# Optimization experiments

Measured on AMD Instinct MI355X. Metric: run time of the kernel, lower is better.

## Reference

```python
import jax, jax.numpy as jnp
import numpy as np

N_DRUG, N_DIS = 3072, 3072
N = N_DRUG + N_DIS
E = 196608
F1, F2, F3 = 512, 256, 128
GAMMA1 = GAMMA2 = GAMMA3 = 0.03125
NEG_SLOPE = 0.2   # GATConv default negative_slope
KERNEL_W = 0.25   # drug_ps/dis_ps = 1/kernel_len


def gat_layer(x, src, dst, w_e, W, a_src, a_dst, b):
    """Single-head GATConv: gather -> per-node softmax -> scatter-aggregate.
    Edge weights w_e scale the unnormalized attention."""
    xw = x @ W                                                  # [N, F]
    e = jax.nn.leaky_relu((xw @ a_src)[src] + (xw @ a_dst)[dst], NEG_SLOPE)  # [E]
    m = jax.ops.segment_max(e, dst, num_segments=N)
    ex = jnp.exp(e - m[dst]) * w_e
    denom = jax.ops.segment_sum(ex, dst, num_segments=N)
    alpha = ex / (denom[dst] + 1e-16)
    out = jax.ops.segment_sum(alpha[:, None] * xw[src], dst, num_segments=N)
    return out + b


def gip_kernel(y, gamma):
    """getGipKernel(y, 0, gamma, normalized=True)."""
    mn = jnp.min(y, axis=1, keepdims=True)
    mx = jnp.max(y, axis=1, keepdims=True)
    y = (y - mn) / (mx - mn + 1e-12)          # row-wise min-max normalize
    k = y @ y.T
    k = k / jnp.mean(jnp.diagonal(k))
    d = jnp.diagonal(k)
    dist = d[:, None] + d[None, :] - 2.0 * k  # kernelToDistance
    return jnp.exp(-gamma * dist)


def normalized_kernel(K):
    K = jnp.abs(K)
    minv = jnp.min(jnp.where(K > 0, K, jnp.inf))
    K = jnp.where(K == 0, minv, K)            # replace zeros with min nonzero
    d = jnp.sqrt(jnp.diagonal(K))
    return K / (d[:, None] * d[None, :])


def setup_inputs() -> dict:
    key = jax.random.key(0)
    ks = jax.random.split(key, 20)
    f32 = jnp.float32

    def lin(k, fi, fo):
        return jax.random.normal(k, (fi, fo), f32) * (1.0 / float(np.sqrt(fi)))

    inp = {
        'x': jax.random.normal(ks[0], (N, N), f32),
        'edge_index': jax.random.randint(ks[1], (2, E), 0, N, dtype=jnp.int32),
        'adj_data': jax.random.uniform(ks[2], (N, N), f32),
        'drug_sim': jax.random.uniform(ks[3], (N_DRUG, N_DRUG), f32),
        'dis_sim': jax.random.uniform(ks[4], (N_DIS, N_DIS), f32),
        'alpha1': jax.random.normal(ks[5], (N_DRUG, N_DIS), f32),
        'alpha2': jax.random.normal(ks[6], (N_DIS, N_DRUG), f32),
        'W1': lin(ks[7], N, F1),
        'as1': jax.random.normal(ks[8], (F1,), f32) * 0.1,
        'ad1': jax.random.normal(ks[9], (F1,), f32) * 0.1,
        'b1': jnp.zeros((F1,), f32),
        'W2': lin(ks[10], F1, F2),
        'as2': jax.random.normal(ks[11], (F2,), f32) * 0.1,
        'ad2': jax.random.normal(ks[12], (F2,), f32) * 0.1,
        'b2': jnp.zeros((F2,), f32),
        'W3': lin(ks[13], F2, F3),
        'as3': jax.random.normal(ks[14], (F3,), f32) * 0.1,
        'ad3': jax.random.normal(ks[15], (F3,), f32) * 0.1,
        'b3': jnp.zeros((F3,), f32),
    }
    return inp


def reference(x, edge_index, adj_data, drug_sim, dis_sim, alpha1, alpha2,
              W1, as1, ad1, b1, W2, as2, ad2, b2, W3, as3, ad3, b3):
    src0, dst0 = edge_index[0], edge_index[1]
    w0 = adj_data[src0, dst0]                  # per-edge gather of dense weights
    loop = jnp.arange(N, dtype=src0.dtype)     # GATConv add_self_loops=True
    src = jnp.concatenate([src0, loop])
    dst = jnp.concatenate([dst0, loop])
    w = jnp.concatenate([w0, jnp.ones((N,), adj_data.dtype)])

    H1 = jax.nn.relu(gat_layer(x, src, dst, w, W1, as1, ad1, b1))
    H2 = jax.nn.relu(gat_layer(H1, src, dst, w, W2, as2, ad2, b2))
    H3 = jax.nn.relu(gat_layer(H2, src, dst, w, W3, as3, ad3, b3))

    drug_k = KERNEL_W * (gip_kernel(H1[:N_DRUG], GAMMA1)
                         + gip_kernel(H2[:N_DRUG], GAMMA2)
                         + gip_kernel(H3[:N_DRUG], GAMMA3) + drug_sim)
    dis_k = KERNEL_W * (gip_kernel(H1[N_DRUG:], GAMMA1)
                        + gip_kernel(H2[N_DRUG:], GAMMA2)
                        + gip_kernel(H3[N_DRUG:], GAMMA3) + dis_sim)

    out1 = normalized_kernel(drug_k) @ alpha1  # [N_DRUG, N_DIS]
    out2 = normalized_kernel(dis_k) @ alpha2   # [N_DIS, N_DRUG]
    return 0.5 * (out1 + out2.T)
```

## Files before the change

### kernel.cpp

```cpp
#include <hip/hip_runtime.h>
#include <hip/hip_bf16.h>
#include <stdint.h>

#define N_NODES 6144
#define N_DRUG  3072
#define N_EDGE  196608
#define E_TOT   (N_EDGE + N_NODES)
#define GAMMA   0.03125f
#define LOG2E   1.44269504f

typedef __bf16 bf16x8 __attribute__((ext_vector_type(8)));
typedef float  f32x4  __attribute__((ext_vector_type(4)));

__device__ __forceinline__ unsigned short f2b(float f){
  union { float f; unsigned u; } v; v.f = f;
  unsigned r = v.u + 0x7FFFu + ((v.u >> 16) & 1u);
  return (unsigned short)(r >> 16);
}
__device__ __forceinline__ float b2f(unsigned short b){
  union { unsigned u; float f; } v; v.u = ((unsigned)b) << 16;
  return v.f;
}
__device__ __forceinline__ float fexp2(float x){
  float r; asm("v_exp_f32 %0, %1" : "=v"(r) : "v"(x)); return r;
}
__device__ __forceinline__ void gl_lds(const void* g, void* l){
  __builtin_amdgcn_global_load_lds((const __attribute__((address_space(1))) void*)g,
                                   (__attribute__((address_space(3))) void*)l, 16, 0, 0);
}

#define WAITVM(N) asm volatile("s_waitcnt vmcnt(" #N ")" ::: "memory")
#define SYNC() { __builtin_amdgcn_sched_barrier(0); __builtin_amdgcn_s_barrier(); __builtin_amdgcn_sched_barrier(0); }

__global__ void cast_bf16_k(const float* __restrict__ in, unsigned short* __restrict__ out, long n){
  long i = ((long)blockIdx.x*blockDim.x + threadIdx.x)*4;
  long stride = (long)gridDim.x*blockDim.x*4;
  for (; i < n; i += stride){
    float4 v = *(const float4*)(in + i);
    ushort4 o;
    o.x = f2b(v.x); o.y = f2b(v.y); o.z = f2b(v.z); o.w = f2b(v.w);
    *(ushort4*)(out + i) = o;
  }
}

__global__ void tcast_k(const float* __restrict__ in, unsigned short* __restrict__ out,
                        int R, int Cd, int OLD, int OOFF){
  __shared__ float tile[32][33];
  int bx = blockIdx.x*32, by = blockIdx.y*32;
  int tx = threadIdx.x, ty = threadIdx.y;
  for (int i = ty; i < 32; i += 8) tile[i][tx] = in[(long)(by+i)*Cd + bx + tx];
  __syncthreads();
  for (int i = ty; i < 32; i += 8) out[(long)(bx+i)*OLD + OOFF + by + tx] = f2b(tile[tx][i]);
}

__global__ void tcast2_k(const float* __restrict__ a2, const float* __restrict__ a1,
                         unsigned short* __restrict__ o0, unsigned short* __restrict__ o1){
  __shared__ float tile[32][33];
  const float* in = blockIdx.z ? a1 : a2;
  unsigned short* out = blockIdx.z ? o1 : o0;
  int OOFF = blockIdx.z ? 0 : N_DRUG;
  int bx = blockIdx.x*32, by = blockIdx.y*32;
  int tx = threadIdx.x, ty = threadIdx.y;
  for (int i = ty; i < 32; i += 8) tile[i][tx] = in[(long)(by+i)*N_DRUG + bx + tx];
  __syncthreads();
  for (int i = ty; i < 32; i += 8) out[(long)(bx+i)*N_NODES + OOFF + by + tx] = f2b(tile[tx][i]);
}

__global__ void hist_k(const int* __restrict__ ei, int* __restrict__ cnt){
  int i = blockIdx.x*blockDim.x + threadIdx.x;
  if (i >= E_TOT) return;
  int d = (i < N_EDGE) ? ei[N_EDGE + i] : (i - N_EDGE);
  atomicAdd(&cnt[d], 1);
}

__global__ void scan_k(const int* __restrict__ cnt, int* __restrict__ ptr){
  __shared__ int sums[1024];
  int t = threadIdx.x;
  int v[6]; int s = 0;
  #pragma unroll
  for (int i = 0; i < 6; i++){ v[i] = s; s += cnt[t*6 + i]; }
  sums[t] = s; __syncthreads();
  for (int off = 1; off < 1024; off <<= 1){
    int add = (t >= off) ? sums[t - off] : 0;
    __syncthreads();
    sums[t] += add;
    __syncthreads();
  }
  int base = (t == 0) ? 0 : sums[t-1];
  #pragma unroll
  for (int i = 0; i < 6; i++) ptr[t*6 + i] = base + v[i];
  if (t == 1023) ptr[N_NODES] = sums[1023];
}

__global__ void scatter_k(const int* __restrict__ ei, const float* __restrict__ adj,
                          const int* __restrict__ ptr, int* __restrict__ cur,
                          int* __restrict__ srcs, int* __restrict__ dsts,
                          float* __restrict__ wcsr){
  int i = blockIdx.x*blockDim.x + threadIdx.x;
  if (i >= E_TOT) return;
  int s = (i < N_EDGE) ? ei[i] : (i - N_EDGE);
  int d = (i < N_EDGE) ? ei[N_EDGE + i] : (i - N_EDGE);
  int pos = ptr[d] + atomicAdd(&cur[d], 1);
  srcs[pos] = s; dsts[pos] = d;
  wcsr[pos] = (i < N_EDGE) ? adj[(long)s*N_NODES + d] : 1.0f;
}

__global__ void dots_k(const unsigned short* __restrict__ XWb, const float* __restrict__ av,
                       const float* __restrict__ dv, float* __restrict__ es,
                       float* __restrict__ ed, int F){
  int n = blockIdx.x, l = threadIdx.x;
  float s = 0.f, d = 0.f;
  for (int f = l*4; f < F; f += 256){
    ushort4 u = *(const ushort4*)(XWb + (long)n*F + f);
    float4 a = *(const float4*)(av + f);
    float4 dd = *(const float4*)(dv + f);
    s += b2f(u.x)*a.x + b2f(u.y)*a.y + b2f(u.z)*a.z + b2f(u.w)*a.w;
    d += b2f(u.x)*dd.x + b2f(u.y)*dd.y + b2f(u.z)*dd.z + b2f(u.w)*dd.w;
  }
  #pragma unroll
  for (int off = 32; off > 0; off >>= 1){ s += __shfl_down(s, off); d += __shfl_down(d, off); }
  if (l == 0){ es[n] = s; ed[n] = d; }
}

__global__ void phase12_k(const int* __restrict__ srcs, const int* __restrict__ dsts,
                          const float* __restrict__ wcsr,
                          const float* __restrict__ es, const float* __restrict__ ed,
                          float* __restrict__ exc){
  int p = blockIdx.x*blockDim.x + threadIdx.x;
  if (p >= E_TOT) return;
  int s = srcs[p], d = dsts[p];
  float e = es[s] + ed[d];
  e = (e > 0.f) ? e : 0.2f*e;
  exc[p] = fexp2(e * LOG2E) * wcsr[p];
}

__global__ void agg4_k(const unsigned short* __restrict__ XWb, const int* __restrict__ ptr,
                       const int* __restrict__ srcs, const float* __restrict__ exc,
                       const float* __restrict__ bias,
                       unsigned short* __restrict__ Hb, int F){
  int n = blockIdx.x, t = threadIdx.x;
  int st = ptr[n], en = ptr[n+1];
  float a0v = 0.f, a1v = 0.f, a2v = 0.f, a3v = 0.f, dsum = 0.f;
  int j = st;
  for (; j + 1 < en; j += 2){
    float w0 = exc[j], w1 = exc[j+1];
    int s0 = srcs[j], s1 = srcs[j+1];
    ushort4 u0 = *(const ushort4*)(XWb + (long)s0*F + t*4);
    ushort4 u1 = *(const ushort4*)(XWb + (long)s1*F + t*4);
    dsum += w0 + w1;
    a0v += w0*b2f(u0.x) + w1*b2f(u1.x); a1v += w0*b2f(u0.y) + w1*b2f(u1.y);
    a2v += w0*b2f(u0.z) + w1*b2f(u1.z); a3v += w0*b2f(u0.w) + w1*b2f(u1.w);
  }
  if (j < en){
    float w0 = exc[j]; int s0 = srcs[j];
    ushort4 u0 = *(const ushort4*)(XWb + (long)s0*F + t*4);
    dsum += w0;
    a0v += w0*b2f(u0.x); a1v += w0*b2f(u0.y); a2v += w0*b2f(u0.z); a3v += w0*b2f(u0.w);
  }
  float invd = 1.f/(dsum + 1e-16f);
  float4 b = *(const float4*)(bias + t*4);
  ushort4 ob;
  ob.x = f2b(fmaxf(a0v*invd + b.x, 0.f)); ob.y = f2b(fmaxf(a1v*invd + b.y, 0.f));
  ob.z = f2b(fmaxf(a2v*invd + b.z, 0.f)); ob.w = f2b(fmaxf(a3v*invd + b.w, 0.f));
  *(ushort4*)(Hb + (long)n*F + t*4) = ob;
}

__global__ void agg_k(const unsigned short* __restrict__ XWb, const int* __restrict__ ptr,
                      const int* __restrict__ srcs, const float* __restrict__ exc,
                      const float* __restrict__ bias,
                      unsigned short* __restrict__ Hb, int F){
  int n = blockIdx.x, t = threadIdx.x;
  int st = ptr[n], en = ptr[n+1];
  float ax = 0.f, ay = 0.f, dsum = 0.f;
  int j = st;
  for (; j + 1 < en; j += 2){
    float a0 = exc[j], a1 = exc[j+1];
    int s0 = srcs[j], s1 = srcs[j+1];
    ushort2 u0 = *(const ushort2*)(XWb + (long)s0*F + t*2);
    ushort2 u1 = *(const ushort2*)(XWb + (long)s1*F + t*2);
    dsum += a0 + a1;
    ax += a0*b2f(u0.x) + a1*b2f(u1.x);
    ay += a0*b2f(u0.y) + a1*b2f(u1.y);
  }
  if (j < en){
    float a = exc[j]; int s = srcs[j];
    ushort2 u = *(const ushort2*)(XWb + (long)s*F + t*2);
    dsum += a;
    ax += a*b2f(u.x); ay += a*b2f(u.y);
  }
  float invd = 1.f/(dsum + 1e-16f);
  float2 b = *(const float2*)(bias + t*2);
  ushort2 o;
  o.x = f2b(fmaxf(ax*invd + b.x, 0.f));
  o.y = f2b(fmaxf(ay*invd + b.y, 0.f));
  *(ushort2*)(Hb + (long)n*F + t*2) = o;
}

__global__ void rownorm_all_k(const unsigned short* __restrict__ H0, const unsigned short* __restrict__ H1,
                              const unsigned short* __restrict__ H2,
                              unsigned short* __restrict__ y0, unsigned short* __restrict__ y1,
                              float* __restrict__ dv0, float* __restrict__ dv1){
  int seg = blockIdx.y;
  int side = seg / 3, layer = seg % 3;
  int F = 512 >> layer;
  const unsigned short* H = (layer == 0) ? H0 : (layer == 1) ? H1 : H2;
  H += (size_t)(side ? N_DRUG : 0) * F;
  unsigned short* yb = ((side ? y1 : y0) + ((layer == 0) ? 0 : (layer == 1) ? 512 : 768));
  float* dvec = (side ? dv1 : dv0) + layer*N_DRUG;

  int r = blockIdx.x, t = threadIdx.x;
  __shared__ float ra[256], rb[256];
  float mn = 3.4e38f, mx = -3.4e38f;
  for (int f = t; f < F; f += 256){
    float v = b2f(H[(long)r*F + f]);
    mn = fminf(mn, v); mx = fmaxf(mx, v);
  }
  ra[t] = mn; rb[t] = mx; __syncthreads();
  for (int s2 = 128; s2 > 0; s2 >>= 1){
    if (t < s2){ ra[t] = fminf(ra[t], ra[t+s2]); rb[t] = fmaxf(rb[t], rb[t+s2]); }
    __syncthreads();
  }
  mn = ra[0]; mx = rb[0];
  __syncthreads();
  float sc = 1.f/(mx - mn + 1e-12f);
  float s = 0.f;
  for (int f = t; f < F; f += 256){
    float v = (b2f(H[(long)r*F + f]) - mn)*sc;
    unsigned short b = f2b(v);
    yb[(long)r*896 + f] = b;
    float vb = b2f(b);
    s += vb*vb;
  }
  ra[t] = s; __syncthreads();
  for (int s2 = 128; s2 > 0; s2 >>= 1){
    if (t < s2) ra[t] += ra[t+s2];
    __syncthreads();
  }
  if (t == 0) dvec[r] = ra[0];
}

__global__ void vsum_diag_k(const float* __restrict__ dv0, const float* __restrict__ dv1,
                            float* __restrict__ sump,
                            const float* __restrict__ sim0, const float* __restrict__ sim1,
                            float* __restrict__ rs0, float* __restrict__ rs1){
  int y = blockIdx.y;
  int t = threadIdx.x;
  if (y < 6){
    int side = y / 3, layer = y % 3;
    const float* v = (side ? dv1 : dv0) + layer*N_DRUG;
    __shared__ float red[256];
    float s = 0.f;
    for (int i = blockIdx.x*256 + t; i < N_DRUG; i += gridDim.x*256) s += v[i];
    red[t] = s; __syncthreads();
    for (int s2 = 128; s2 > 0; s2 >>= 1){ if (t < s2) red[t] += red[t+s2]; __syncthreads(); }
    if (t == 0) atomicAdd(&sump[y], red[0]);
  } else {
    int side = y - 6;
    int i = blockIdx.x*256 + t;
    const float* sim = side ? sim1 : sim0;
    float* rs = side ? rs1 : rs0;
    if (i < N_DRUG) rs[i] = rsqrtf(sim[(long)i*N_DRUG + i] + 3.0f);
  }
}

__global__ __launch_bounds__(512, 2) void gemm8p(
    const unsigned short* __restrict__ A, const unsigned short* __restrict__ Bt,
    float* __restrict__ P, float* __restrict__ Palt, int M, int N, int K, int kz)
{
  __shared__ unsigned short lds[2][2][16384];
  int t = threadIdx.x;
  int lane = t & 63, wave = t >> 6;
  int wm = wave >> 2, wn = wave & 3;

  int nbx = gridDim.x;
  int nwg = nbx * gridDim.y;
  int bid = blockIdx.y * nbx + blockIdx.x;
  int cpx = nwg >> 3;
  int swz = (bid & 7) * cpx + (bid >> 3);
  long brow = (long)(swz / nbx) * 256;
  long bcol = (long)(swz % nbx) * 256;
  long k0 = (long)blockIdx.z * kz;
  int nt = kz >> 6;

  int sr = wave*8 + (lane >> 3);
  int cg = (lane & 7) ^ (lane >> 3);
  const unsigned short* gA = A  + (brow + sr)*(long)K + k0 + cg*8;
  const unsigned short* gB = Bt + (bcol + sr)*(long)K + k0 + cg*8;
  unsigned ldsw = wave * 512;

  auto stage = [&](int b, int mat, int h, int tk){
    const unsigned short* g = (mat ? gB : gA) + (long)(h*128)*K + (long)tk*64;
    unsigned short* d = &lds[b][mat][h*8192 + ldsw];
    gl_lds(g, d);
    gl_lds(g + (long)64*K, d + 4096);
  };

  int fr = lane & 15, q = lane >> 4;
  int lo = fr*64 + ((q ^ (fr & 7))*8);
  int dk = (lo ^ 32) - lo;

  f32x4 acc[8][4];
  #pragma unroll
  for (int a = 0; a < 8; a++)
    #pragma unroll
    for (int b = 0; b < 4; b++){ acc[a][b][0]=0.f; acc[a][b][1]=0.f; acc[a][b][2]=0.f; acc[a][b][3]=0.f; }
  bf16x8 af[4][2], bf[4][2];

  const unsigned short* a0p = &lds[0][0][wm*8192 + lo];
  const unsigned short* b0p = &lds[0][1][wn*4096 + lo];
  const unsigned short* a1p = &lds[1][0][wm*8192 + lo];
  const unsigned short* b1p = &lds[1][1][wn*4096 + lo];

#define RD_AF_LO(ab) { _Pragma("unroll") for (int j = 0; j < 4; ++j){ \
    af[j][0] = *(const bf16x8*)((ab) + j*1024); af[j][1] = *(const bf16x8*)((ab) + j*1024 + dk); } }
#define RD_AF_HI(ab) { _Pragma("unroll") for (int j = 0; j < 4; ++j){ \
    af[j][0] = *(const bf16x8*)((ab) + (4+j)*1024); af[j][1] = *(const bf16x8*)((ab) + (4+j)*1024 + dk); } }
#define RD_BF_LO(bb) { _Pragma("unroll") for (int j = 0; j < 2; ++j){ \
    bf[j][0] = *(const bf16x8*)((bb) + j*1024); bf[j][1] = *(const bf16x8*)((bb) + j*1024 + dk); } }
#define RD_BF_HI(bb) { _Pragma("unroll") for (int j = 2; j < 4; ++j){ \
    bf[j][0] = *(const bf16x8*)((bb) + j*1024); bf[j][1] = *(const bf16x8*)((bb) + j*1024 + dk); } }
#define MFMA_Q(MB, NB) { __builtin_amdgcn_s_setprio(1); \
    _Pragma("unroll") for (int kk = 0; kk < 2; ++kk) \
      _Pragma("unroll") for (int mi = 0; mi < 4; ++mi) \
        _Pragma("unroll") for (int ni = (NB); ni < (NB)+2; ++ni) \
          acc[(MB)+mi][ni] = __builtin_amdgcn_mfma_f32_16x16x32_bf16(af[mi][kk], bf[ni][kk], acc[(MB)+mi][ni], 0, 0, 0); \
    __builtin_amdgcn_s_setprio(0); }

  stage(0,0,0,0); stage(0,0,1,0); stage(0,1,0,0); stage(0,1,1,0);
  stage(1,1,0,1); stage(1,1,1,1);
  WAITVM(4);
  SYNC();

  int half = nt >> 1;
  for (int i = 0; i < half; ++i){
    int t1 = 2*i+1, t2 = 2*i+2, t3 = 2*i+3;
    bool s2 = t2 < nt, s3 = t3 < nt;
    RD_AF_LO(a0p); RD_BF_LO(b0p);
    stage(1,0,0,t1);
    SYNC(); MFMA_Q(0,0); SYNC();
    RD_BF_HI(b0p);
    stage(1,0,1,t1);
    SYNC(); MFMA_Q(0,2); SYNC();
    RD_AF_HI(a0p);
    if (s2) stage(0,1,0,t2);
    SYNC(); MFMA_Q(4,0); SYNC();
    if (s2){ stage(0,1,1,t2); WAITVM(4); } else { WAITVM(0); }
    SYNC(); MFMA_Q(4,2); SYNC();
    RD_AF_LO(a1p); RD_BF_LO(b1p);
    if (s2) stage(0,0,0,t2);
    SYNC(); MFMA_Q(0,0); SYNC();
    RD_BF_HI(b1p);
    if (s2) stage(0,0,1,t2);
    SYNC(); MFMA_Q(0,2); SYNC();
    RD_AF_HI(a1p);
    if (s3) stage(1,1,0,t3);
    SYNC(); MFMA_Q(4,0); SYNC();
    if (s3){ stage(1,1,1,t3); WAITVM(4); } else { WAITVM(0); }
    SYNC(); MFMA_Q(4,2); SYNC();
  }
#undef RD_AF_LO
#undef RD_AF_HI
#undef RD_BF_LO
#undef RD_BF_HI
#undef MFMA_Q

  int z = blockIdx.z;
  float* Pz = (z < 2) ? (P + (long)z*M*N) : (Palt + (long)(z-2)*M*N);
  #pragma unroll
  for (int mi = 0; mi < 8; ++mi){
    #pragma unroll
    for (int ni = 0; ni < 4; ++ni){
      long col = bcol + wn*64 + ni*16 + fr;
      #pragma unroll
      for (int r = 0; r < 4; ++r){
        long row = brow + wm*128 + mi*16 + q*4 + r;
        Pz[row*N + col] = acc[mi][ni][r];
      }
    }
  }
}

__global__ void reduce4b_k(const float* __restrict__ p, unsigned short* __restrict__ outb, long n){
  long i = ((long)blockIdx.x*blockDim.x + threadIdx.x)*4;
  if (i >= n) return;
  float4 s = *(const float4*)(p + i);
  #pragma unroll
  for (int z = 1; z < 4; z++){
    float4 x = *(const float4*)(p + (long)z*n + i);
    s.x += x.x; s.y += x.y; s.z += x.z; s.w += x.w;
  }
  ushort4 o; o.x = f2b(s.x); o.y = f2b(s.y); o.z = f2b(s.z); o.w = f2b(s.w);
  *(ushort4*)(outb + i) = o;
}

__global__ void reduce3h_k(const float* __restrict__ pa, const float* __restrict__ pb,
                           const float* __restrict__ pc, float* __restrict__ out, long n){
  long i = ((long)blockIdx.x*blockDim.x + threadIdx.x)*4;
  if (i >= n) return;
  float4 a = *(const float4*)(pa + i);
  float4 b = *(const float4*)(pb + i);
  float4 c = *(const float4*)(pc + i);
  float4 o;
  o.x = 0.5f*(a.x + b.x + c.x); o.y = 0.5f*(a.y + b.y + c.y);
  o.z = 0.5f*(a.z + b.z + c.z); o.w = 0.5f*(a.w + b.w + c.w);
  *(float4*)(out + i) = o;
}

__global__ __launch_bounds__(256) void gemm_tn(
    const unsigned short* __restrict__ A, const unsigned short* __restrict__ Bt,
    unsigned short* __restrict__ Cb, int M, int N, int K)
{
  __shared__ unsigned short As[2][128*64];
  __shared__ unsigned short Bs[2][128*64];
  int t = threadIdx.x;
  int wave = t >> 6, lane = t & 63;
  int brow = blockIdx.y*128, bcol = blockIdx.x*128;
  int wr = (wave >> 1)*64, wc = (wave & 1)*64;
  int fr = lane & 15, q = lane >> 4;
  int rin = lane >> 3, kslot = (lane & 7) ^ rin;

  f32x4 acc[4][4];
  #pragma unroll
  for (int a = 0; a < 4; a++)
    #pragma unroll
    for (int b = 0; b < 4; b++){ acc[a][b][0]=0.f; acc[a][b][1]=0.f; acc[a][b][2]=0.f; acc[a][b][3]=0.f; }

  int aoff[4][2], boff[4][2];
  #pragma unroll
  for (int mi = 0; mi < 4; mi++){
    int row = wr + mi*16 + fr;
    #pragma unroll
    for (int kk = 0; kk < 2; kk++) aoff[mi][kk] = row*64 + (((kk*4 + q) ^ (row & 7))*8);
  }
  #pragma unroll
  for (int ni = 0; ni < 4; ni++){
    int row = wc + ni*16 + fr;
    #pragma unroll
    for (int kk = 0; kk < 2; kk++) boff[ni][kk] = row*64 + (((kk*4 + q) ^ (row & 7))*8);
  }

  auto stage = [&](int buf, int k0){
    #pragma unroll
    for (int p = 0; p < 4; p++){
      int rsec = p*32 + wave*8;
      gl_lds(A  + (long)(brow + rsec + rin)*K + k0 + kslot*8, &As[buf][rsec*64]);
      gl_lds(Bt + (long)(bcol + rsec + rin)*K + k0 + kslot*8, &Bs[buf][rsec*64]);
    }
  };

  int nsteps = K >> 6;
  stage(0, 0);
  __syncthreads();
  int curb = 0;
  for (int s = 0; s < nsteps; s++){
    if (s + 1 < nsteps) stage(curb ^ 1, (s + 1)*64);
    const unsigned short* a_l = As[curb];
    const unsigned short* b_l = Bs[curb];
    #pragma unroll
    for (int kk = 0; kk < 2; kk++){
      bf16x8 af[4], bfv[4];
      #pragma unroll
      for (int mi = 0; mi < 4; mi++) af[mi]  = *(const bf16x8*)(a_l + aoff[mi][kk]);
      #pragma unroll
      for (int ni = 0; ni < 4; ni++) bfv[ni] = *(const bf16x8*)(b_l + boff[ni][kk]);
      #pragma unroll
      for (int mi = 0; mi < 4; mi++)
        #pragma unroll
        for (int ni = 0; ni < 4; ni++)
          acc[mi][ni] = __builtin_amdgcn_mfma_f32_16x16x32_bf16(af[mi], bfv[ni], acc[mi][ni], 0, 0, 0);
    }
    __syncthreads();
    curb ^= 1;
  }

  #pragma unroll
  for (int mi = 0; mi < 4; mi++){
    #pragma unroll
    for (int ni = 0; ni < 4; ni++){
      int col = bcol + wc + ni*16 + fr;
      #pragma unroll
      for (int r = 0; r < 4; r++){
        int row = brow + wr + mi*16 + q*4 + r;
        Cb[(long)row*N + col] = f2b(acc[mi][ni][r]);
      }
    }
  }
}

__global__ __launch_bounds__(512) void gip_gemm(
    const unsigned short* __restrict__ Y0, const unsigned short* __restrict__ Y1,
    const float* __restrict__ sim0, const float* __restrict__ sim1,
    const float* __restrict__ dva, const float* __restrict__ dvb,
    const float* __restrict__ sumps,
    const float* __restrict__ rs0, const float* __restrict__ rs1,
    unsigned short* __restrict__ o0, unsigned short* __restrict__ o1)
{
  __shared__ unsigned short As[2][128*64];
  __shared__ unsigned short Bs[2][128*64];
  const int K = 896;
  int side = blockIdx.z;
  const unsigned short* Y = side ? Y1 : Y0;
  const float* sim  = side ? sim1 : sim0;
  const float* dv   = side ? dvb : dva;
  const float* sums = sumps + side*3;
  const float* rs   = side ? rs1 : rs0;
  unsigned short* outp = side ? o1 : o0;
  int outoff = side ? N_DRUG : 0;

  int t = threadIdx.x;
  int wave = t >> 6, lane = t & 63;
  int brow = blockIdx.y*128, bcol = blockIdx.x*128;
  int wr = (wave >> 1)*32, wc = (wave & 1)*64;
  int fr = lane & 15, q = lane >> 4;
  int rin = lane >> 3, kslot = (lane & 7) ^ rin;

  f32x4 acc0[2][4], acc1[2][4], acc2[2][4];
  #pragma unroll
  for (int a = 0; a < 2; a++)
    #pragma unroll
    for (int b = 0; b < 4; b++){
      acc0[a][b][0]=0.f;acc0[a][b][1]=0.f;acc0[a][b][2]=0.f;acc0[a][b][3]=0.f;
      acc1[a][b][0]=0.f;acc1[a][b][1]=0.f;acc1[a][b][2]=0.f;acc1[a][b][3]=0.f;
      acc2[a][b][0]=0.f;acc2[a][b][1]=0.f;acc2[a][b][2]=0.f;acc2[a][b][3]=0.f;
    }

  int aoff[2][2], boff[4][2];
  #pragma unroll
  for (int mi = 0; mi < 2; mi++){
    int row = wr + mi*16 + fr;
    #pragma unroll
    for (int kk = 0; kk < 2; kk++) aoff[mi][kk] = row*64 + (((kk*4 + q) ^ (row & 7))*8);
  }
  #pragma unroll
  for (int ni = 0; ni < 4; ni++){
    int row = wc + ni*16 + fr;
    #pragma unroll
    for (int kk = 0; kk < 2; kk++) boff[ni][kk] = row*64 + (((kk*4 + q) ^ (row & 7))*8);
  }

  auto stage = [&](int buf, int k0){
    #pragma unroll
    for (int p = 0; p < 2; p++){
      int rsec = p*64 + wave*8;
      gl_lds(Y + (long)(brow + rsec + rin)*K + k0 + kslot*8, &As[buf][rsec*64]);
      gl_lds(Y + (long)(bcol + rsec + rin)*K + k0 + kslot*8, &Bs[buf][rsec*64]);
    }
  };

  int curb = 0, s = 0;
  stage(0, 0);
  __syncthreads();

#define GSTEP(ACC) { \
    if (s + 1 < 14) stage(curb ^ 1, (s + 1)*64); \
    const unsigned short* a_l = As[curb]; \
    const unsigned short* b_l = Bs[curb]; \
    _Pragma("unroll") \
    for (int kk = 0; kk < 2; kk++){ \
      bf16x8 af0 = *(const bf16x8*)(a_l + aoff[0][kk]); \
      bf16x8 af1 = *(const bf16x8*)(a_l + aoff[1][kk]); \
      _Pragma("unroll") \
      for (int ni = 0; ni < 4; ni++){ \
        bf16x8 bv = *(const bf16x8*)(b_l + boff[ni][kk]); \
        ACC[0][ni] = __builtin_amdgcn_mfma_f32_16x16x32_bf16(af0, bv, ACC[0][ni], 0, 0, 0); \
        ACC[1][ni] = __builtin_amdgcn_mfma_f32_16x16x32_bf16(af1, bv, ACC[1][ni], 0, 0, 0); \
      } \
    } \
    __syncthreads(); curb ^= 1; s++; }

  for (int i = 0; i < 8; i++) GSTEP(acc0)
  for (int i = 0; i < 4; i++) GSTEP(acc1)
  for (int i = 0; i < 2; i++) GSTEP(acc2)
#undef GSTEP

  float h0 = GAMMA * ((float)N_DRUG / sums[0]) * LOG2E;
  float h1 = GAMMA * ((float)N_DRUG / sums[1]) * LOG2E;
  float h2 = GAMMA * ((float)N_DRUG / sums[2]) * LOG2E;
  float c0 = 2.f*h0, c1 = 2.f*h1, c2 = 2.f*h2;
  #pragma unroll
  for (int mi = 0; mi < 2; mi++){
    #pragma unroll
    for (int ni = 0; ni < 4; ni++){
      int col = bcol + wc + ni*16 + fr;
      float d0c = dv[col], d1c = dv[N_DRUG + col], d2c = dv[2*N_DRUG + col];
      float rc = rs[col];
      #pragma unroll
      for (int r = 0; r < 4; r++){
        int row = brow + wr + mi*16 + q*4 + r;
        float b0 = -h0*(dv[row] + d0c);
        float b1 = -h1*(dv[N_DRUG + row] + d1c);
        float b2 = -h2*(dv[2*N_DRUG + row] + d2c);
        float v = sim[(long)row*N_DRUG + col]
                + fexp2(fmaf(c0, acc0[mi][ni][r], b0))
                + fexp2(fmaf(c1, acc1[mi][ni][r], b1))
                + fexp2(fmaf(c2, acc2[mi][ni][r], b2));
        outp[(long)row*N_NODES + outoff + col] = f2b(v * rs[row] * rc);
      }
    }
  }
}

extern "C" void kernel_launch(void* const* d_in, const int* in_sizes, int n_in,
                              void* d_out, int out_size, void* d_ws, size_t ws_size,
                              hipStream_t stream){
  const float* x        = (const float*)d_in[0];
  const int*   ei       = (const int*)d_in[1];
  const float* adj      = (const float*)d_in[2];
  const float* drug_sim = (const float*)d_in[3];
  const float* dis_sim  = (const float*)d_in[4];
  const float* alpha1   = (const float*)d_in[5];
  const float* alpha2   = (const float*)d_in[6];
  const float* W[3]   = {(const float*)d_in[7],  (const float*)d_in[11], (const float*)d_in[15]};
  const float* as_[3] = {(const float*)d_in[8],  (const float*)d_in[12], (const float*)d_in[16]};
  const float* ad_[3] = {(const float*)d_in[9],  (const float*)d_in[13], (const float*)d_in[17]};
  const float* bs_[3] = {(const float*)d_in[10], (const float*)d_in[14], (const float*)d_in[18]};
  float* out = (float*)d_out;
  const int Fs[3] = {512, 256, 128};

  char* p = (char*)d_ws;
  auto alloc = [&](size_t bytes)->char*{
    char* r = p; p += (bytes + 255) & ~(size_t)255; return r;
  };
  unsigned short* xb  = (unsigned short*)alloc((size_t)N_NODES*N_NODES*2);
  unsigned short* wb  = (unsigned short*)alloc((size_t)N_NODES*512*2);
  unsigned short* XWb = (unsigned short*)alloc((size_t)N_NODES*512*2);
  unsigned short* HbL[3];
  HbL[0] = (unsigned short*)alloc((size_t)N_NODES*512*2);
  HbL[1] = (unsigned short*)alloc((size_t)N_NODES*256*2);
  HbL[2] = (unsigned short*)alloc((size_t)N_NODES*128*2);
  float* es    = (float*)alloc(N_NODES*4);
  float* edv   = (float*)alloc(N_NODES*4);
  float* exc   = (float*)alloc((size_t)E_TOT*4);
  int* cntcur  = (int*)alloc((size_t)2*N_NODES*4);
  int* cnt = cntcur, *cur = cntcur + N_NODES;
  int* cptr = (int*)alloc((N_NODES+1)*4);
  int* srcs  = (int*)alloc((size_t)E_TOT*4);
  int* dsts  = (int*)alloc((size_t)E_TOT*4);
  float* wcsr = (float*)alloc((size_t)E_TOT*4);
  unsigned short* ycat[2];
  ycat[0] = (unsigned short*)alloc((size_t)N_DRUG*896*2);
  ycat[1] = (unsigned short*)alloc((size_t)N_DRUG*896*2);
  float* dvv[2];
  dvv[0] = (float*)alloc((size_t)3*N_DRUG*4);
  dvv[1] = (float*)alloc((size_t)3*N_DRUG*4);
  float* sump = (float*)alloc(256);
  float* rsv[2];
  rsv[0] = (float*)alloc(N_DRUG*4);
  rsv[1] = (float*)alloc(N_DRUG*4);
  unsigned short* Abuf  = (unsigned short*)alloc((size_t)N_DRUG*N_NODES*2);
  unsigned short* Btbuf = (unsigned short*)alloc((size_t)N_DRUG*N_NODES*2);

  float* pL1 = (float*)Abuf;
  float* pF01 = (float*)xb;
  float* pF2  = (float*)wb;
  const long MN = (long)N_DRUG*N_DRUG;

  cast_bf16_k<<<4096, 256, 0, stream>>>(x, xb, (long)N_NODES*N_NODES);
  hipMemsetAsync(cntcur, 0, (size_t)2*N_NODES*4, stream);
  hist_k<<<(E_TOT+255)/256, 256, 0, stream>>>(ei, cnt);
  scan_k<<<1, 1024, 0, stream>>>(cnt, cptr);
  scatter_k<<<(E_TOT+255)/256, 256, 0, stream>>>(ei, adj, cptr, cur, srcs, dsts, wcsr);

  const unsigned short* Ain = xb;
  int Kin = N_NODES;
  for (int l = 0; l < 3; l++){
    int F = Fs[l];
    tcast_k<<<dim3(F/32, Kin/32), dim3(32,8), 0, stream>>>(W[l], wb, Kin, F, Kin, 0);
    if (l == 0){
      gemm8p<<<dim3(F/256, N_NODES/256, 4), 512, 0, stream>>>(Ain, wb, pL1, pL1 + 2*(long)N_NODES*F, N_NODES, F, Kin, Kin/4);
      reduce4b_k<<<(int)(((long)N_NODES*F/4 + 255)/256), 256, 0, stream>>>(pL1, XWb, (long)N_NODES*F);
    } else {
      gemm_tn<<<dim3(F/128, N_NODES/128), 256, 0, stream>>>(Ain, wb, XWb, N_NODES, F, Kin);
    }
    dots_k<<<N_NODES, 64, 0, stream>>>(XWb, as_[l], ad_[l], es, edv, F);
    phase12_k<<<(E_TOT+255)/256, 256, 0, stream>>>(srcs, dsts, wcsr, es, edv, exc);
    if (F >= 256)
      agg4_k<<<N_NODES, F/4, 0, stream>>>(XWb, cptr, srcs, exc, bs_[l], HbL[l], F);
    else
      agg_k<<<N_NODES, 64, 0, stream>>>(XWb, cptr, srcs, exc, bs_[l], HbL[l], F);
    Ain = HbL[l]; Kin = F;
  }

  hipMemsetAsync(sump, 0, 24, stream);
  rownorm_all_k<<<dim3(N_DRUG, 6), 256, 0, stream>>>(HbL[0], HbL[1], HbL[2],
                                                     ycat[0], ycat[1], dvv[0], dvv[1]);
  vsum_diag_k<<<dim3(12, 8), 256, 0, stream>>>(dvv[0], dvv[1], sump,
                                               drug_sim, dis_sim, rsv[0], rsv[1]);

  tcast2_k<<<dim3(N_DRUG/32, N_DRUG/32, 2), dim3(32,8), 0, stream>>>(alpha2, alpha1, Abuf, Btbuf);

  gip_gemm<<<dim3(N_DRUG/128, N_DRUG/128, 2), 512, 0, stream>>>(
      ycat[0], ycat[1], drug_sim, dis_sim, dvv[0], dvv[1], sump, rsv[0], rsv[1], Abuf, Btbuf);

  gemm8p<<<dim3(N_DRUG/256, N_DRUG/256, 3), 512, 0, stream>>>(Abuf, Btbuf, pF01, pF2, N_DRUG, N_DRUG, N_NODES, N_NODES/3);
  reduce3h_k<<<(int)((MN/4 + 255)/256), 256, 0, stream>>>(pF01, pF01 + MN, pF2, out, MN);

  (void)in_sizes; (void)n_in; (void)out_size; (void)ws_size;
}
```

Before: 562.0 us.

## Fuse edge attention scoring into aggregation kernels and drop dsts array

Removes the separate per-edge phase12 kernel. Attention weights are now computed inside the aggregation kernels from es/ed and the CSR edge weights, so the dsts and exc arrays are no longer stored. The vsum reduction is rewritten to use a single block per segment with a direct store, which removes a memset and the atomics. pF2 gets its own buffer instead of aliasing wb. The cost is that exp is recomputed by every thread in each aggregation block, and the vsum reduction runs on fewer blocks.

```diff
diff --git a/kernel.cpp b/kernel.cpp
--- a/kernel.cpp
+++ b/kernel.cpp
@@ -94,14 +94,13 @@
 
 __global__ void scatter_k(const int* __restrict__ ei, const float* __restrict__ adj,
                           const int* __restrict__ ptr, int* __restrict__ cur,
-                          int* __restrict__ srcs, int* __restrict__ dsts,
-                          float* __restrict__ wcsr){
+                          int* __restrict__ srcs, float* __restrict__ wcsr){
   int i = blockIdx.x*blockDim.x + threadIdx.x;
   if (i >= E_TOT) return;
   int s = (i < N_EDGE) ? ei[i] : (i - N_EDGE);
   int d = (i < N_EDGE) ? ei[N_EDGE + i] : (i - N_EDGE);
   int pos = ptr[d] + atomicAdd(&cur[d], 1);
-  srcs[pos] = s; dsts[pos] = d;
+  srcs[pos] = s;
   wcsr[pos] = (i < N_EDGE) ? adj[(long)s*N_NODES + d] : 1.0f;
 }
 
@@ -122,29 +121,22 @@
   if (l == 0){ es[n] = s; ed[n] = d; }
 }
 
-__global__ void phase12_k(const int* __restrict__ srcs, const int* __restrict__ dsts,
-                          const float* __restrict__ wcsr,
-                          const float* __restrict__ es, const float* __restrict__ ed,
-                          float* __restrict__ exc){
-  int p = blockIdx.x*blockDim.x + threadIdx.x;
-  if (p >= E_TOT) return;
-  int s = srcs[p], d = dsts[p];
-  float e = es[s] + ed[d];
-  e = (e > 0.f) ? e : 0.2f*e;
-  exc[p] = fexp2(e * LOG2E) * wcsr[p];
-}
-
 __global__ void agg4_k(const unsigned short* __restrict__ XWb, const int* __restrict__ ptr,
-                       const int* __restrict__ srcs, const float* __restrict__ exc,
+                       const int* __restrict__ srcs, const float* __restrict__ wcsr,
+                       const float* __restrict__ es, const float* __restrict__ ed,
                        const float* __restrict__ bias,
                        unsigned short* __restrict__ Hb, int F){
   int n = blockIdx.x, t = threadIdx.x;
   int st = ptr[n], en = ptr[n+1];
+  float edn = ed[n];
   float a0v = 0.f, a1v = 0.f, a2v = 0.f, a3v = 0.f, dsum = 0.f;
   int j = st;
   for (; j + 1 < en; j += 2){
-    float w0 = exc[j], w1 = exc[j+1];
     int s0 = srcs[j], s1 = srcs[j+1];
+    float e0 = es[s0] + edn; e0 = (e0 > 0.f) ? e0 : 0.2f*e0;
+    float e1 = es[s1] + edn; e1 = (e1 > 0.f) ? e1 : 0.2f*e1;
+    float w0 = fexp2(e0*LOG2E) * wcsr[j];
+    float w1 = fexp2(e1*LOG2E) * wcsr[j+1];
     ushort4 u0 = *(const ushort4*)(XWb + (long)s0*F + t*4);
     ushort4 u1 = *(const ushort4*)(XWb + (long)s1*F + t*4);
     dsum += w0 + w1;
@@ -152,7 +144,9 @@
     a2v += w0*b2f(u0.z) + w1*b2f(u1.z); a3v += w0*b2f(u0.w) + w1*b2f(u1.w);
   }
   if (j < en){
-    float w0 = exc[j]; int s0 = srcs[j];
+    int s0 = srcs[j];
+    float e0 = es[s0] + edn; e0 = (e0 > 0.f) ? e0 : 0.2f*e0;
+    float w0 = fexp2(e0*LOG2E) * wcsr[j];
     ushort4 u0 = *(const ushort4*)(XWb + (long)s0*F + t*4);
     dsum += w0;
     a0v += w0*b2f(u0.x); a1v += w0*b2f(u0.y); a2v += w0*b2f(u0.z); a3v += w0*b2f(u0.w);
@@ -166,16 +160,21 @@
 }
 
 __global__ void agg_k(const unsigned short* __restrict__ XWb, const int* __restrict__ ptr,
-                      const int* __restrict__ srcs, const float* __restrict__ exc,
+                      const int* __restrict__ srcs, const float* __restrict__ wcsr,
+                      const float* __restrict__ es, const float* __restrict__ ed,
                       const float* __restrict__ bias,
                       unsigned short* __restrict__ Hb, int F){
   int n = blockIdx.x, t = threadIdx.x;
   int st = ptr[n], en = ptr[n+1];
+  float edn = ed[n];
   float ax = 0.f, ay = 0.f, dsum = 0.f;
   int j = st;
   for (; j + 1 < en; j += 2){
-    float a0 = exc[j], a1 = exc[j+1];
     int s0 = srcs[j], s1 = srcs[j+1];
+    float e0 = es[s0] + edn; e0 = (e0 > 0.f) ? e0 : 0.2f*e0;
+    float e1 = es[s1] + edn; e1 = (e1 > 0.f) ? e1 : 0.2f*e1;
+    float a0 = fexp2(e0*LOG2E) * wcsr[j];
+    float a1 = fexp2(e1*LOG2E) * wcsr[j+1];
     ushort2 u0 = *(const ushort2*)(XWb + (long)s0*F + t*2);
     ushort2 u1 = *(const ushort2*)(XWb + (long)s1*F + t*2);
     dsum += a0 + a1;
@@ -183,8 +182,10 @@
     ay += a0*b2f(u0.y) + a1*b2f(u1.y);
   }
   if (j < en){
-    float a = exc[j]; int s = srcs[j];
-    ushort2 u = *(const ushort2*)(XWb + (long)s*F + t*2);
+    int s0 = srcs[j];
+    float e0 = es[s0] + edn; e0 = (e0 > 0.f) ? e0 : 0.2f*e0;
+    float a = fexp2(e0*LOG2E) * wcsr[j];
+    ushort2 u = *(const ushort2*)(XWb + (long)s0*F + t*2);
     dsum += a;
     ax += a*b2f(u.x); ay += a*b2f(u.y);
   }
@@ -246,14 +247,15 @@
   int y = blockIdx.y;
   int t = threadIdx.x;
   if (y < 6){
+    if (blockIdx.x != 0) return;
     int side = y / 3, layer = y % 3;
     const float* v = (side ? dv1 : dv0) + layer*N_DRUG;
     __shared__ float red[256];
     float s = 0.f;
-    for (int i = blockIdx.x*256 + t; i < N_DRUG; i += gridDim.x*256) s += v[i];
+    for (int i = t; i < N_DRUG; i += 256) s += v[i];
     red[t] = s; __syncthreads();
     for (int s2 = 128; s2 > 0; s2 >>= 1){ if (t < s2) red[t] += red[t+s2]; __syncthreads(); }
-    if (t == 0) atomicAdd(&sump[y], red[0]);
+    if (t == 0) sump[y] = red[0];
   } else {
     int side = y - 6;
     int i = blockIdx.x*256 + t;
@@ -630,12 +632,10 @@
   HbL[2] = (unsigned short*)alloc((size_t)N_NODES*128*2);
   float* es    = (float*)alloc(N_NODES*4);
   float* edv   = (float*)alloc(N_NODES*4);
-  float* exc   = (float*)alloc((size_t)E_TOT*4);
   int* cntcur  = (int*)alloc((size_t)2*N_NODES*4);
   int* cnt = cntcur, *cur = cntcur + N_NODES;
   int* cptr = (int*)alloc((N_NODES+1)*4);
   int* srcs  = (int*)alloc((size_t)E_TOT*4);
-  int* dsts  = (int*)alloc((size_t)E_TOT*4);
   float* wcsr = (float*)alloc((size_t)E_TOT*4);
   unsigned short* ycat[2];
   ycat[0] = (unsigned short*)alloc((size_t)N_DRUG*896*2);
@@ -649,17 +649,17 @@
   rsv[1] = (float*)alloc(N_DRUG*4);
   unsigned short* Abuf  = (unsigned short*)alloc((size_t)N_DRUG*N_NODES*2);
   unsigned short* Btbuf = (unsigned short*)alloc((size_t)N_DRUG*N_NODES*2);
+  float* pF2 = (float*)alloc((size_t)N_DRUG*N_DRUG*4);
 
   float* pL1 = (float*)Abuf;
   float* pF01 = (float*)xb;
-  float* pF2  = (float*)wb;
   const long MN = (long)N_DRUG*N_DRUG;
 
   cast_bf16_k<<<4096, 256, 0, stream>>>(x, xb, (long)N_NODES*N_NODES);
   hipMemsetAsync(cntcur, 0, (size_t)2*N_NODES*4, stream);
   hist_k<<<(E_TOT+255)/256, 256, 0, stream>>>(ei, cnt);
   scan_k<<<1, 1024, 0, stream>>>(cnt, cptr);
-  scatter_k<<<(E_TOT+255)/256, 256, 0, stream>>>(ei, adj, cptr, cur, srcs, dsts, wcsr);
+  scatter_k<<<(E_TOT+255)/256, 256, 0, stream>>>(ei, adj, cptr, cur, srcs, wcsr);
 
   const unsigned short* Ain = xb;
   int Kin = N_NODES;
@@ -673,15 +673,13 @@
       gemm_tn<<<dim3(F/128, N_NODES/128), 256, 0, stream>>>(Ain, wb, XWb, N_NODES, F, Kin);
     }
     dots_k<<<N_NODES, 64, 0, stream>>>(XWb, as_[l], ad_[l], es, edv, F);
-    phase12_k<<<(E_TOT+255)/256, 256, 0, stream>>>(srcs, dsts, wcsr, es, edv, exc);
     if (F >= 256)
-      agg4_k<<<N_NODES, F/4, 0, stream>>>(XWb, cptr, srcs, exc, bs_[l], HbL[l], F);
+      agg4_k<<<N_NODES, F/4, 0, stream>>>(XWb, cptr, srcs, wcsr, es, edv, bs_[l], HbL[l], F);
     else
-      agg_k<<<N_NODES, 64, 0, stream>>>(XWb, cptr, srcs, exc, bs_[l], HbL[l], F);
+      agg_k<<<N_NODES, 64, 0, stream>>>(XWb, cptr, srcs, wcsr, es, edv, bs_[l], HbL[l], F);
     Ain = HbL[l]; Kin = F;
   }
 
-  hipMemsetAsync(sump, 0, 24, stream);
   rownorm_all_k<<<dim3(N_DRUG, 6), 256, 0, stream>>>(HbL[0], HbL[1], HbL[2],
                                                      ycat[0], ycat[1], dvv[0], dvv[1]);
   vsum_diag_k<<<dim3(12, 8), 256, 0, stream>>>(dvv[0], dvv[1], sump,
```

New measurement: 557.6 us. About the same (-0.8%).
